# Performance work log

Hardware: AMD Instinct MI355X
Metric: run time of the kernel (lower is better)

## Reference

```python
import jax, jax.numpy as jnp
import numpy as np

MUL = 32            # multiplicity of 0e and 1o irreps
IN_DIM = MUL * 4    # 32 scalars + 32 vectors = 128
SH_DIM = 4          # 1x0e + 1x1o
N_EDGE_FEAT = 128
HIDDEN = 128
W_NUMEL = 4 * MUL * MUL  # 4 CG paths, uvw weights 32x1x32 each
EPS = 1e-5
INV_SQRT3 = 1.0 / np.sqrt(3.0)
PATH_NORM = 1.0 / np.sqrt(2.0 * MUL)  # 2 paths per output irrep, fan-in MUL


def _fc(edge_attr, W1, b1, W2, b2):
    h = jax.nn.relu(edge_attr @ W1 + b1)
    return h @ W2 + b2  # [E, W_NUMEL]


def _tensor_product(x, sh, w):
    # FullyConnectedTensorProduct for (32x0e+32x1o) x (1x0e+1x1o) -> (32x0e+32x1o)
    # CG (real w3j): 0x0->0: 1 ; 0x1->1, 1x0->1, 1x1->0: delta/sqrt(3)
    E = x.shape[0]
    x0 = x[:, :MUL]                      # [E,32]   scalars
    x1 = x[:, MUL:].reshape(E, MUL, 3)   # [E,32,3] vectors
    sh0 = sh[:, 0]                       # [E]
    sh1 = sh[:, 1:4]                     # [E,3]
    wA = w[:, 0 * MUL * MUL:1 * MUL * MUL].reshape(E, MUL, MUL)  # 0e x 0e -> 0e
    wB = w[:, 1 * MUL * MUL:2 * MUL * MUL].reshape(E, MUL, MUL)  # 0e x 1o -> 1o
    wC = w[:, 2 * MUL * MUL:3 * MUL * MUL].reshape(E, MUL, MUL)  # 1o x 0e -> 1o
    wD = w[:, 3 * MUL * MUL:4 * MUL * MUL].reshape(E, MUL, MUL)  # 1o x 1o -> 0e
    out0 = PATH_NORM * (
        jnp.einsum('eu,euw->ew', x0 * sh0[:, None], wA)
        + INV_SQRT3 * jnp.einsum('eui,ei,euw->ew', x1, sh1, wD))
    out1 = PATH_NORM * INV_SQRT3 * (
        jnp.einsum('eu,ei,euw->ewi', x0, sh1, wB)
        + jnp.einsum('eui,euw->ewi', x1 * sh0[:, None, None], wC))
    return jnp.concatenate([out0, out1.reshape(E, MUL * 3)], axis=-1)  # [E,128]


def _batch_norm(x, bn_weight, bn_bias):
    # e3nn-style equivariant BatchNorm (training stats): scalars get mean/var
    # normalization + affine; vectors get norm normalization + scale.
    N = x.shape[0]
    s = x[:, :MUL]                       # [N,32]
    v = x[:, MUL:].reshape(N, MUL, 3)    # [N,32,3]
    s = s - s.mean(axis=0)
    s = s * (jax.lax.rsqrt((s ** 2).mean(axis=0) + EPS) * bn_weight[:MUL]) + bn_bias
    v_norm = jax.lax.rsqrt((v ** 2).mean(axis=-1).mean(axis=0) + EPS)  # [32]
    v = v * (v_norm * bn_weight[MUL:])[None, :, None]
    return jnp.concatenate([s, v.reshape(N, MUL * 3)], axis=-1)


def _forward(node_attr, edge_index, edge_attr, edge_sh,
             W1, b1, W2, b2, bn_weight, bn_bias):
    edge_src, edge_dst = edge_index[0], edge_index[1]
    N = node_attr.shape[0]
    w = _fc(edge_attr, W1, b1, W2, b2)                     # [E, 4096]
    tp = _tensor_product(node_attr[edge_dst], edge_sh, w)  # [E, 128]
    # scatter mean over edge_src
    summed = jax.ops.segment_sum(tp, edge_src, num_segments=N)
    counts = jax.ops.segment_sum(jnp.ones((tp.shape[0],), tp.dtype), edge_src,
                                 num_segments=N)
    out = summed / jnp.maximum(counts, 1.0)[:, None]
    out = out + node_attr                                  # residual (same dim, pad=0)
    return _batch_norm(out, bn_weight, bn_bias)


def setup_inputs() -> dict:
    key = jax.random.key(0)
    ks = jax.random.split(key, 10)
    N, E = 10000, 60000
    node_attr = jax.random.normal(ks[0], (N, IN_DIM), jnp.float32)
    edge_index = jax.random.randint(ks[1], (2, E), 0, N)
    edge_attr = jax.random.normal(ks[2], (E, N_EDGE_FEAT), jnp.float32)
    edge_sh = jax.random.normal(ks[3], (E, SH_DIM), jnp.float32)
    W1 = jax.random.normal(ks[4], (N_EDGE_FEAT, HIDDEN), jnp.float32) / np.sqrt(N_EDGE_FEAT)
    b1 = jnp.zeros((HIDDEN,), jnp.float32)
    W2 = jax.random.normal(ks[5], (HIDDEN, W_NUMEL), jnp.float32) / np.sqrt(HIDDEN)
    b2 = jnp.zeros((W_NUMEL,), jnp.float32)
    bn_weight = jnp.ones((2 * MUL,), jnp.float32)
    bn_bias = jnp.zeros((MUL,), jnp.float32)
    return {"node_attr": node_attr, "edge_index": edge_index,
            "edge_attr": edge_attr, "edge_sh": edge_sh,
            "W1": W1, "b1": b1, "W2": W2, "b2": b2,
            "bn_weight": bn_weight, "bn_bias": bn_bias}


def reference(node_attr, edge_index, edge_attr, edge_sh,
              W1, b1, W2, b2, bn_weight, bn_bias):
    return _forward(node_attr, edge_index, edge_attr, edge_sh,
                    W1, b1, W2, b2, bn_weight, bn_bias)
```

## Files before the change

kernel.cpp:

```cpp
#include <hip/hip_runtime.h>
#include <math.h>

#define EPSV 1e-5f
#define IS3  0.57735026918962576f
#define PNRM 0.125f

typedef __attribute__((ext_vector_type(8)))  short  short8;
typedef __attribute__((ext_vector_type(16))) float  floatx16;

static __device__ inline unsigned short f2bf(float f) {
    unsigned int u = __float_as_uint(f);
    return (unsigned short)((u + 0x7fff + ((u >> 16) & 1)) >> 16);
}
static __device__ inline float bflo(unsigned int u) { return __uint_as_float(u << 16); }
static __device__ inline float bfhi(unsigned int u) { return __uint_as_float(u & 0xffff0000u); }

#define GLD16(gp, lp) __builtin_amdgcn_global_load_lds( \
    (const __attribute__((address_space(1))) unsigned int*)(gp), \
    (__attribute__((address_space(3))) unsigned int*)(lp), 16, 0, 0)

__global__ __launch_bounds__(256) void k0_sw(const float* __restrict__ src,
                                             unsigned short* __restrict__ dst,
                                             int total, int ncShift, int ncMask) {
    int i = blockIdx.x * 256 + threadIdx.x;
    if (i >= total) return;
    int k = i >> ncShift, c = i & ncMask;
    dst[(size_t)(c >> 5) * 4096 + (k >> 3) * 256 + (c & 31) * 8 + (k & 7)] = f2bf(src[i]);
}

__global__ __launch_bounds__(256) void k1_fc(const float* __restrict__ ea,
                                             const unsigned short* __restrict__ W1T,
                                             const float* __restrict__ b1,
                                             const int* __restrict__ ei,
                                             unsigned short* __restrict__ h,
                                             int* __restrict__ deg, int E) {
    __shared__ __align__(16) unsigned short W1s[16384];
    const int tid = threadIdx.x, lane = tid & 63, wv = tid >> 6;
    const int half = lane >> 5, col = lane & 31;
    const int e0 = blockIdx.x * 128;

    if (tid < 128) { int e = e0 + tid; if (e < E) atomicAdd(&deg[ei[e]], 1); }

#pragma unroll
    for (int q = 0; q < 8; ++q) {
        int chunk = wv * 8 + q;
        GLD16((const char*)W1T + chunk * 1024 + lane * 16, (char*)W1s + chunk * 1024);
    }

    int e = e0 + wv * 32 + col; if (e >= E) e = E - 1;
    short8 afr[8];
#pragma unroll
    for (int c = 0; c < 8; ++c) {
        const float4* p = (const float4*)(ea + (size_t)e * 128 + c * 16 + half * 8);
        float4 f0 = p[0], f1 = p[1];
        short8 v;
        v[0] = (short)f2bf(f0.x); v[1] = (short)f2bf(f0.y);
        v[2] = (short)f2bf(f0.z); v[3] = (short)f2bf(f0.w);
        v[4] = (short)f2bf(f1.x); v[5] = (short)f2bf(f1.y);
        v[6] = (short)f2bf(f1.z); v[7] = (short)f2bf(f1.w);
        afr[c] = v;
    }
    __syncthreads();

#pragma unroll
    for (int jt = 0; jt < 4; ++jt) {
        floatx16 d = {0,0,0,0,0,0,0,0,0,0,0,0,0,0,0,0};
#pragma unroll
        for (int c = 0; c < 8; ++c) {
            short8 bf = *(const short8*)((const char*)W1s + jt * 8192 + (2 * c + half) * 512 + col * 16);
            d = __builtin_amdgcn_mfma_f32_32x32x16_bf16(afr[c], bf, d, 0, 0, 0);
        }
        int j = jt * 32 + col;
        float b1v = b1[j];
#pragma unroll
        for (int reg = 0; reg < 16; ++reg) {
            int r = (reg & 3) + 8 * (reg >> 2) + 4 * half;
            int er = e0 + wv * 32 + r;
            if (er < E) {
                float v = d[reg] + b1v;
                v = v > 0.f ? v : 0.f;
                h[(size_t)er * 128 + j] = f2bf(v);
            }
        }
    }
}

__global__ __launch_bounds__(256, 2) void k2_mfma(const unsigned short* __restrict__ h,
                                                  const unsigned short* __restrict__ W2T,
                                                  const float* __restrict__ b2,
                                                  const float* __restrict__ na,
                                                  const int* __restrict__ ei,
                                                  const float* __restrict__ sh,
                                                  float* __restrict__ tp, int E) {
    __shared__ __align__(16) char smem[74752];
    unsigned short* As  = (unsigned short*)smem;
    unsigned short* Bs0 = (unsigned short*)(smem + 16384);
    unsigned short* Bs1 = (unsigned short*)(smem + 32768);
    unsigned short* Ctb = (unsigned short*)(smem + 49152);
    float* shs = (float*)(smem + 73728);
    float* red = (float*)smem;

    const int tid = threadIdx.x, lane = tid & 63, wv = tid >> 6;
    const int half = lane >> 5, col = lane & 31;
    const int ust = wv >> 1, esub = wv & 1;
    const int e0 = blockIdx.x * 64;

    if (tid < 64) {
        int e = e0 + tid; int ec = e < E ? e : E - 1;
        float4 s = *(const float4*)(sh + (size_t)ec * 4);
        *(float4*)&shs[tid * 4] = s;
    }

    for (int idx = tid; idx < 2048; idx += 256) {
        int el = idx & 63, u = idx >> 6;
        int e = e0 + el; int ec = e < E ? e : E - 1;
        int dn = ei[E + ec];
        const float* nar = na + (size_t)dn * 128;
        float x0  = nar[u];
        float x10 = nar[32 + u * 3], x11 = nar[33 + u * 3], x12 = nar[34 + u * 3];
        const float* shr = sh + (size_t)ec * 4;
        float s0 = shr[0], s1 = shr[1], s2 = shr[2], s3 = shr[3];
        int o = u * 64 + el;
        Ctb[0 * 2048 + o] = f2bf(x0 * s0);
        Ctb[1 * 2048 + o] = f2bf(x0);
        Ctb[2 * 2048 + o] = f2bf(x10);
        Ctb[3 * 2048 + o] = f2bf(x11);
        Ctb[4 * 2048 + o] = f2bf(x12);
        Ctb[5 * 2048 + o] = f2bf(IS3 * (x10 * s1 + x11 * s2 + x12 * s3));
    }

#pragma unroll
    for (int q = 0; q < 4; ++q) {
        int t = wv * 4 + q;
        int g = t >> 3;
        int jj = (t & 7) * 64 + lane;
        int e = e0 + g * 32 + (jj & 31); int ec = e < E ? e : E - 1;
        GLD16((const char*)h + (size_t)ec * 256 + (jj >> 5) * 16,
              (char*)As + g * 8192 + (t & 7) * 1024);
    }
#pragma unroll
    for (int q = 0; q < 4; ++q) {
        int chunk = wv * 4 + q;
        GLD16((const char*)W2T + chunk * 1024 + lane * 16, (char*)Bs0 + chunk * 1024);
    }
    __syncthreads();

    short8 afr[8];
#pragma unroll
    for (int c = 0; c < 8; ++c)
        afr[c] = *(const short8*)((const char*)As + esub * 8192 + (2 * c + half) * 512 + col * 16);

    float acc0[16] = {}, accB[16] = {}, accC0[16] = {}, accC1[16] = {}, accC2[16] = {};

    for (int p = 0; p < 64; ++p) {
        if (p < 63) {
            char* dst = ((p + 1) & 1) ? (char*)Bs1 : (char*)Bs0;
#pragma unroll
            for (int q = 0; q < 4; ++q) {
                int chunk = wv * 4 + q;
                GLD16((const char*)W2T + (p + 1) * 16384 + chunk * 1024 + lane * 16,
                      dst + chunk * 1024);
            }
        }
        const int ct = 2 * p + ust;
        const int b = ct >> 5, u = ct & 31;
        const char* bb = ((p & 1) ? (const char*)Bs1 : (const char*)Bs0) + ust * 8192;

        floatx16 d = {0,0,0,0,0,0,0,0,0,0,0,0,0,0,0,0};
#pragma unroll
        for (int c = 0; c < 8; ++c) {
            short8 bf = *(const short8*)(bb + (2 * c + half) * 512 + col * 16);
            d = __builtin_amdgcn_mfma_f32_32x32x16_bf16(afr[c], bf, d, 0, 0, 0);
        }
        float b2v = b2[ct * 32 + col];

        const int elb0 = esub * 32 + half * 4;
        if (b == 0 || b == 3) {
            const unsigned short* tb = Ctb + (b == 0 ? 0 : 5) * 2048;
#pragma unroll
            for (int q = 0; q < 4; ++q) {
                uint2 cv = *(const uint2*)&tb[u * 64 + elb0 + q * 8];
                acc0[q * 4 + 0] += bflo(cv.x) * (d[q * 4 + 0] + b2v);
                acc0[q * 4 + 1] += bfhi(cv.x) * (d[q * 4 + 1] + b2v);
                acc0[q * 4 + 2] += bflo(cv.y) * (d[q * 4 + 2] + b2v);
                acc0[q * 4 + 3] += bfhi(cv.y) * (d[q * 4 + 3] + b2v);
            }
        } else if (b == 1) {
#pragma unroll
            for (int q = 0; q < 4; ++q) {
                uint2 cv = *(const uint2*)&Ctb[1 * 2048 + u * 64 + elb0 + q * 8];
                accB[q * 4 + 0] += bflo(cv.x) * (d[q * 4 + 0] + b2v);
                accB[q * 4 + 1] += bfhi(cv.x) * (d[q * 4 + 1] + b2v);
                accB[q * 4 + 2] += bflo(cv.y) * (d[q * 4 + 2] + b2v);
                accB[q * 4 + 3] += bfhi(cv.y) * (d[q * 4 + 3] + b2v);
            }
        } else {
#pragma unroll
            for (int q = 0; q < 4; ++q) {
                uint2 c0 = *(const uint2*)&Ctb[2 * 2048 + u * 64 + elb0 + q * 8];
                uint2 c1 = *(const uint2*)&Ctb[3 * 2048 + u * 64 + elb0 + q * 8];
                uint2 c2 = *(const uint2*)&Ctb[4 * 2048 + u * 64 + elb0 + q * 8];
#pragma unroll
                for (int rr = 0; rr < 4; ++rr) {
                    float v = d[q * 4 + rr] + b2v;
                    float f0 = (rr == 0) ? bflo(c0.x) : (rr == 1) ? bfhi(c0.x) : (rr == 2) ? bflo(c0.y) : bfhi(c0.y);
                    float f1 = (rr == 0) ? bflo(c1.x) : (rr == 1) ? bfhi(c1.x) : (rr == 2) ? bflo(c1.y) : bfhi(c1.y);
                    float f2 = (rr == 0) ? bflo(c2.x) : (rr == 1) ? bfhi(c2.x) : (rr == 2) ? bflo(c2.y) : bfhi(c2.y);
                    accC0[q * 4 + rr] += f0 * v;
                    accC1[q * 4 + rr] += f1 * v;
                    accC2[q * 4 + rr] += f2 * v;
                }
            }
        }
        __syncthreads();
    }

    if (ust == 1) {
#pragma unroll
        for (int reg = 0; reg < 16; ++reg) {
            red[(((esub * 5 + 0) * 16 + reg) << 6) + lane] = acc0[reg];
            red[(((esub * 5 + 1) * 16 + reg) << 6) + lane] = accB[reg];
            red[(((esub * 5 + 2) * 16 + reg) << 6) + lane] = accC0[reg];
            red[(((esub * 5 + 3) * 16 + reg) << 6) + lane] = accC1[reg];
            red[(((esub * 5 + 4) * 16 + reg) << 6) + lane] = accC2[reg];
        }
    }
    __syncthreads();
    if (ust == 0) {
#pragma unroll
        for (int q = 0; q < 4; ++q) {
#pragma unroll
            for (int rr = 0; rr < 4; ++rr) {
                int reg = q * 4 + rr;
                int el = esub * 32 + q * 8 + half * 4 + rr;
                int e = e0 + el;
                if (e >= E) continue;
                float a0 = acc0[reg] + red[(((esub * 5 + 0) * 16 + reg) << 6) + lane];
                float aB = accB[reg] + red[(((esub * 5 + 1) * 16 + reg) << 6) + lane];
                float c0v = accC0[reg] + red[(((esub * 5 + 2) * 16 + reg) << 6) + lane];
                float c1v = accC1[reg] + red[(((esub * 5 + 3) * 16 + reg) << 6) + lane];
                float c2v = accC2[reg] + red[(((esub * 5 + 4) * 16 + reg) << 6) + lane];
                float4 sv = *(const float4*)&shs[el * 4];
                float* tpe = tp + (size_t)e * 128;
                tpe[col] = PNRM * a0;
                tpe[32 + col * 3 + 0] = PNRM * IS3 * (sv.y * aB + sv.x * c0v);
                tpe[32 + col * 3 + 1] = PNRM * IS3 * (sv.z * aB + sv.x * c1v);
                tpe[32 + col * 3 + 2] = PNRM * IS3 * (sv.w * aB + sv.x * c2v);
            }
        }
    }
}

__global__ __launch_bounds__(1024) void k_scan(const int* __restrict__ deg,
                                               int* __restrict__ rowptr, int N) {
    __shared__ int part[1024];
    const int tid = threadIdx.x;
    const int chunk = (N + 1023) / 1024;
    const int base = tid * chunk;
    int s = 0;
    for (int i = 0; i < chunk; ++i) {
        int n = base + i;
        if (n < N) s += deg[n];
    }
    part[tid] = s;
    __syncthreads();
    for (int off = 1; off < 1024; off <<= 1) {
        int t = 0;
        if (tid >= off) t = part[tid - off];
        __syncthreads();
        if (tid >= off) part[tid] += t;
        __syncthreads();
    }
    int prefix = (tid == 0) ? 0 : part[tid - 1];
    for (int i = 0; i < chunk; ++i) {
        int n = base + i;
        if (n < N) { rowptr[n] = prefix; prefix += deg[n]; }
    }
    if (tid == 0) rowptr[N] = part[1023];
}

__global__ __launch_bounds__(256) void k_fill(const int* __restrict__ ei,
                                              const int* __restrict__ rowptr,
                                              int* __restrict__ cursor,
                                              int* __restrict__ elist, int E) {
    int e = blockIdx.x * 256 + threadIdx.x;
    if (e >= E) return;
    int s = ei[e];
    int pos = rowptr[s] + atomicAdd(&cursor[s], 1);
    elist[pos] = e;
}

__global__ __launch_bounds__(256) void k4_gather(const float* __restrict__ tp,
                                                 const int* __restrict__ rowptr,
                                                 const int* __restrict__ elist,
                                                 const float* __restrict__ na,
                                                 float* __restrict__ pre,
                                                 float* __restrict__ stats, int N) {
    __shared__ float bns[96];
    const int tid = threadIdx.x;
    if (tid < 96) bns[tid] = 0.f;
    __syncthreads();
    const int o = tid & 127, hf = tid >> 7;
    for (int n = blockIdx.x * 2 + hf; n < N; n += gridDim.x * 2) {
        int r0 = rowptr[n], r1 = rowptr[n + 1];
        float s = 0.f;
        for (int j = r0; j < r1; ++j)
            s += tp[(size_t)elist[j] * 128 + o];
        int dg = r1 - r0;
        float cf = (float)(dg > 0 ? dg : 1);
        float v = s / cf + na[(size_t)n * 128 + o];
        pre[(size_t)n * 128 + o] = v;
        if (o < 32) {
            atomicAdd(&bns[o], v);
            atomicAdd(&bns[32 + o], v * v);
        } else {
            atomicAdd(&bns[64 + (o - 32) / 3], v * v);
        }
    }
    __syncthreads();
    if (tid < 96) atomicAdd(&stats[tid], bns[tid]);
}

__global__ __launch_bounds__(256) void k5_bn(const float* __restrict__ pre,
                                             const float* __restrict__ stats,
                                             const float* __restrict__ bnw,
                                             const float* __restrict__ bnb,
                                             float* __restrict__ out, int N) {
    size_t idx = (size_t)blockIdx.x * 256 + threadIdx.x;
    if (idx >= (size_t)N * 128) return;
    int o = (int)(idx & 127);
    float v = pre[idx];
    float invN = 1.f / (float)N;
    if (o < 32) {
        float m   = stats[o] * invN;
        float var = stats[32 + o] * invN - m * m;
        out[idx] = (v - m) * rsqrtf(var + EPSV) * bnw[o] + bnb[o];
    } else {
        int j = (o - 32) / 3;
        float vn = rsqrtf(stats[64 + j] * invN * (1.f / 3.f) + EPSV);
        out[idx] = v * vn * bnw[32 + j];
    }
}

extern "C" void kernel_launch(void* const* d_in, const int* in_sizes, int n_in,
                              void* d_out, int out_size, void* d_ws, size_t ws_size,
                              hipStream_t stream) {
    const float* node_attr  = (const float*)d_in[0];
    const int*   edge_index = (const int*)d_in[1];
    const float* edge_attr  = (const float*)d_in[2];
    const float* edge_sh    = (const float*)d_in[3];
    const float* W1  = (const float*)d_in[4];
    const float* b1  = (const float*)d_in[5];
    const float* W2  = (const float*)d_in[6];
    const float* b2  = (const float*)d_in[7];
    const float* bnw = (const float*)d_in[8];
    const float* bnb = (const float*)d_in[9];

    const int N = in_sizes[0] / 128;
    const int E = in_sizes[1] / 2;

    float* tp     = (float*)d_ws;
    float* pre    = tp + (size_t)E * 128;
    float* stats  = pre + (size_t)N * 128;
    int*   deg    = (int*)(stats + 96);
    int*   cursor = deg + N;
    int*   rowptr = cursor + N;
    int*   elist  = rowptr + N + 1;
    char* pbase = (char*)(elist + E);
    pbase += (16 - ((size_t)pbase & 15)) & 15;
    unsigned short* h   = (unsigned short*)pbase;
    unsigned short* W2T = h + (size_t)E * 128;
    unsigned short* W1T = W2T + (size_t)524288;

    hipMemsetAsync(stats, 0, (96 + 2 * (size_t)N) * sizeof(int), stream);

    k0_sw<<<(128 * 4096 + 255) / 256, 256, 0, stream>>>(W2, W2T, 128 * 4096, 12, 4095);
    k0_sw<<<(128 * 128 + 255) / 256, 256, 0, stream>>>(W1, W1T, 128 * 128, 7, 127);
    k1_fc<<<(E + 127) / 128, 256, 0, stream>>>(edge_attr, W1T, b1, edge_index, h, deg, E);
    k_scan<<<1, 1024, 0, stream>>>(deg, rowptr, N);
    k_fill<<<(E + 255) / 256, 256, 0, stream>>>(edge_index, rowptr, cursor, elist, E);
    k2_mfma<<<(E + 63) / 64, 256, 0, stream>>>(h, W2T, b2, node_attr, edge_index,
                                               edge_sh, tp, E);
    k4_gather<<<256, 256, 0, stream>>>(tp, rowptr, elist, node_attr, pre, stats, N);
    size_t ntot = (size_t)N * 128;
    k5_bn<<<(int)((ntot + 255) / 256), 256, 0, stream>>>(pre, stats, bnw, bnb,
                                                         (float*)d_out, N);
}
```

Before: 317.4 us.

## Stream W2 fragments into registers directly and coalesce weight/hidden stores

The main MFMA kernel stops staging W2 tiles through double-buffered LDS with a per-iteration barrier. Each wave instead loads its B fragments straight from global (L2-resident) memory into registers with a two-deep software pipeline, which cuts LDS from about 73KB to 42KB and drops 64 __syncthreads. The FC kernel stages its output tile in LDS so that h is written as 16-byte rows rather than scattered 2-byte stores, and the weight swizzle kernel now writes its destination contiguously and gathers from the source instead. The cost is more registers for the prefetched fragments and repeated global/L2 reads of W2 by every block.

```diff
diff --git a/kernel.cpp b/kernel.cpp
--- a/kernel.cpp
+++ b/kernel.cpp
@@ -21,11 +21,13 @@
 
 __global__ __launch_bounds__(256) void k0_sw(const float* __restrict__ src,
                                              unsigned short* __restrict__ dst,
-                                             int total, int ncShift, int ncMask) {
+                                             int total, int nc) {
     int i = blockIdx.x * 256 + threadIdx.x;
     if (i >= total) return;
-    int k = i >> ncShift, c = i & ncMask;
-    dst[(size_t)(c >> 5) * 4096 + (k >> 3) * 256 + (c & 31) * 8 + (k & 7)] = f2bf(src[i]);
+    int tile = i >> 12, t = i & 4095;
+    int k = ((t >> 8) << 3) | (t & 7);
+    int c = (tile << 5) | ((t >> 3) & 31);
+    dst[i] = f2bf(src[(size_t)k * nc + c]);
 }
 
 __global__ __launch_bounds__(256) void k1_fc(const float* __restrict__ ea,
@@ -35,6 +37,7 @@
                                              unsigned short* __restrict__ h,
                                              int* __restrict__ deg, int E) {
     __shared__ __align__(16) unsigned short W1s[16384];
+    __shared__ __align__(16) unsigned short outT[5120];
     const int tid = threadIdx.x, lane = tid & 63, wv = tid >> 6;
     const int half = lane >> 5, col = lane & 31;
     const int e0 = blockIdx.x * 128;
@@ -70,18 +73,26 @@
             short8 bf = *(const short8*)((const char*)W1s + jt * 8192 + (2 * c + half) * 512 + col * 16);
             d = __builtin_amdgcn_mfma_f32_32x32x16_bf16(afr[c], bf, d, 0, 0, 0);
         }
-        int j = jt * 32 + col;
-        float b1v = b1[j];
+        float b1v = b1[jt * 32 + col];
 #pragma unroll
         for (int reg = 0; reg < 16; ++reg) {
             int r = (reg & 3) + 8 * (reg >> 2) + 4 * half;
-            int er = e0 + wv * 32 + r;
+            float v = d[reg] + b1v;
+            v = v > 0.f ? v : 0.f;
+            outT[(wv * 32 + r) * 40 + col] = f2bf(v);
+        }
+        __syncthreads();
+#pragma unroll
+        for (int ps = 0; ps < 2; ++ps) {
+            int lin = ps * 256 + tid;
+            int row = lin >> 2, c8 = (lin & 3) * 8;
+            int er = e0 + row;
             if (er < E) {
-                float v = d[reg] + b1v;
-                v = v > 0.f ? v : 0.f;
-                h[(size_t)er * 128 + j] = f2bf(v);
+                short8 v = *(const short8*)&outT[row * 40 + c8];
+                *(short8*)(h + (size_t)er * 128 + jt * 32 + c8) = v;
             }
         }
+        __syncthreads();
     }
 }
 
@@ -92,12 +103,10 @@
                                                   const int* __restrict__ ei,
                                                   const float* __restrict__ sh,
                                                   float* __restrict__ tp, int E) {
-    __shared__ __align__(16) char smem[74752];
+    __shared__ __align__(16) char smem[42240];
     unsigned short* As  = (unsigned short*)smem;
-    unsigned short* Bs0 = (unsigned short*)(smem + 16384);
-    unsigned short* Bs1 = (unsigned short*)(smem + 32768);
-    unsigned short* Ctb = (unsigned short*)(smem + 49152);
-    float* shs = (float*)(smem + 73728);
+    unsigned short* Ctb = (unsigned short*)(smem + 16384);
+    float* shs = (float*)(smem + 40960);
     float* red = (float*)smem;
 
     const int tid = threadIdx.x, lane = tid & 63, wv = tid >> 6;
@@ -138,11 +147,6 @@
         GLD16((const char*)h + (size_t)ec * 256 + (jj >> 5) * 16,
               (char*)As + g * 8192 + (t & 7) * 1024);
     }
-#pragma unroll
-    for (int q = 0; q < 4; ++q) {
-        int chunk = wv * 4 + q;
-        GLD16((const char*)W2T + chunk * 1024 + lane * 16, (char*)Bs0 + chunk * 1024);
-    }
     __syncthreads();
 
     short8 afr[8];
@@ -151,70 +155,75 @@
         afr[c] = *(const short8*)((const char*)As + esub * 8192 + (2 * c + half) * 512 + col * 16);
 
     float acc0[16] = {}, accB[16] = {}, accC0[16] = {}, accC1[16] = {}, accC2[16] = {};
-
-    for (int p = 0; p < 64; ++p) {
-        if (p < 63) {
-            char* dst = ((p + 1) & 1) ? (char*)Bs1 : (char*)Bs0;
-#pragma unroll
-            for (int q = 0; q < 4; ++q) {
-                int chunk = wv * 4 + q;
-                GLD16((const char*)W2T + (p + 1) * 16384 + chunk * 1024 + lane * 16,
-                      dst + chunk * 1024);
-            }
-        }
-        const int ct = 2 * p + ust;
-        const int b = ct >> 5, u = ct & 31;
-        const char* bb = ((p & 1) ? (const char*)Bs1 : (const char*)Bs0) + ust * 8192;
-
-        floatx16 d = {0,0,0,0,0,0,0,0,0,0,0,0,0,0,0,0};
-#pragma unroll
-        for (int c = 0; c < 8; ++c) {
-            short8 bf = *(const short8*)(bb + (2 * c + half) * 512 + col * 16);
-            d = __builtin_amdgcn_mfma_f32_32x32x16_bf16(afr[c], bf, d, 0, 0, 0);
-        }
-        float b2v = b2[ct * 32 + col];
-
-        const int elb0 = esub * 32 + half * 4;
-        if (b == 0 || b == 3) {
-            const unsigned short* tb = Ctb + (b == 0 ? 0 : 5) * 2048;
-#pragma unroll
-            for (int q = 0; q < 4; ++q) {
-                uint2 cv = *(const uint2*)&tb[u * 64 + elb0 + q * 8];
-                acc0[q * 4 + 0] += bflo(cv.x) * (d[q * 4 + 0] + b2v);
-                acc0[q * 4 + 1] += bfhi(cv.x) * (d[q * 4 + 1] + b2v);
-                acc0[q * 4 + 2] += bflo(cv.y) * (d[q * 4 + 2] + b2v);
-                acc0[q * 4 + 3] += bfhi(cv.y) * (d[q * 4 + 3] + b2v);
-            }
-        } else if (b == 1) {
-#pragma unroll
-            for (int q = 0; q < 4; ++q) {
-                uint2 cv = *(const uint2*)&Ctb[1 * 2048 + u * 64 + elb0 + q * 8];
-                accB[q * 4 + 0] += bflo(cv.x) * (d[q * 4 + 0] + b2v);
-                accB[q * 4 + 1] += bfhi(cv.x) * (d[q * 4 + 1] + b2v);
-                accB[q * 4 + 2] += bflo(cv.y) * (d[q * 4 + 2] + b2v);
-                accB[q * 4 + 3] += bfhi(cv.y) * (d[q * 4 + 3] + b2v);
-            }
-        } else {
-#pragma unroll
-            for (int q = 0; q < 4; ++q) {
-                uint2 c0 = *(const uint2*)&Ctb[2 * 2048 + u * 64 + elb0 + q * 8];
-                uint2 c1 = *(const uint2*)&Ctb[3 * 2048 + u * 64 + elb0 + q * 8];
-                uint2 c2 = *(const uint2*)&Ctb[4 * 2048 + u * 64 + elb0 + q * 8];
-#pragma unroll
-                for (int rr = 0; rr < 4; ++rr) {
-                    float v = d[q * 4 + rr] + b2v;
-                    float f0 = (rr == 0) ? bflo(c0.x) : (rr == 1) ? bfhi(c0.x) : (rr == 2) ? bflo(c0.y) : bfhi(c0.y);
-                    float f1 = (rr == 0) ? bflo(c1.x) : (rr == 1) ? bfhi(c1.x) : (rr == 2) ? bflo(c1.y) : bfhi(c1.y);
-                    float f2 = (rr == 0) ? bflo(c2.x) : (rr == 1) ? bfhi(c2.x) : (rr == 2) ? bflo(c2.y) : bfhi(c2.y);
-                    accC0[q * 4 + rr] += f0 * v;
-                    accC1[q * 4 + rr] += f1 * v;
-                    accC2[q * 4 + rr] += f2 * v;
-                }
-            }
-        }
-        __syncthreads();
-    }
-
+    const int elb0 = esub * 32 + half * 4;
+    const unsigned short* bbase = W2T + half * 256 + col * 8;
+
+#define LOADB(p, br, b2r) do {                                         \
+        int _ct = 2 * (p) + ust;                                       \
+        const unsigned short* _bp = bbase + (size_t)_ct * 4096;        \
+        _Pragma("unroll")                                              \
+        for (int _c = 0; _c < 8; ++_c)                                 \
+            (br)[_c] = *(const short8*)(_bp + _c * 512);               \
+        (b2r) = b2[_ct * 32 + col];                                    \
+    } while (0)
+
+#define COMPUTE(p, br, b2v) do {                                                              \
+        const int _ct = 2 * (p) + ust;                                                        \
+        const int _b = _ct >> 5, _u = _ct & 31;                                               \
+        floatx16 d = {0,0,0,0,0,0,0,0,0,0,0,0,0,0,0,0};                                       \
+        _Pragma("unroll")                                                                     \
+        for (int _c = 0; _c < 8; ++_c)                                                        \
+            d = __builtin_amdgcn_mfma_f32_32x32x16_bf16(afr[_c], (br)[_c], d, 0, 0, 0);       \
+        if (_b == 0 || _b == 3) {                                                             \
+            const unsigned short* tb = Ctb + (_b == 0 ? 0 : 5) * 2048;                        \
+            _Pragma("unroll")                                                                 \
+            for (int q = 0; q < 4; ++q) {                                                     \
+                uint2 cv = *(const uint2*)&tb[_u * 64 + elb0 + q * 8];                        \
+                acc0[q * 4 + 0] += bflo(cv.x) * (d[q * 4 + 0] + (b2v));                       \
+                acc0[q * 4 + 1] += bfhi(cv.x) * (d[q * 4 + 1] + (b2v));                       \
+                acc0[q * 4 + 2] += bflo(cv.y) * (d[q * 4 + 2] + (b2v));                       \
+                acc0[q * 4 + 3] += bfhi(cv.y) * (d[q * 4 + 3] + (b2v));                       \
+            }                                                                                 \
+        } else if (_b == 1) {                                                                 \
+            _Pragma("unroll")                                                                 \
+            for (int q = 0; q < 4; ++q) {                                                     \
+                uint2 cv = *(const uint2*)&Ctb[1 * 2048 + _u * 64 + elb0 + q * 8];            \
+                accB[q * 4 + 0] += bflo(cv.x) * (d[q * 4 + 0] + (b2v));                       \
+                accB[q * 4 + 1] += bfhi(cv.x) * (d[q * 4 + 1] + (b2v));                       \
+                accB[q * 4 + 2] += bflo(cv.y) * (d[q * 4 + 2] + (b2v));                       \
+                accB[q * 4 + 3] += bfhi(cv.y) * (d[q * 4 + 3] + (b2v));                       \
+            }                                                                                 \
+        } else {                                                                              \
+            _Pragma("unroll")                                                                 \
+            for (int q = 0; q < 4; ++q) {                                                     \
+                uint2 cu0 = *(const uint2*)&Ctb[2 * 2048 + _u * 64 + elb0 + q * 8];           \
+                uint2 cu1 = *(const uint2*)&Ctb[3 * 2048 + _u * 64 + elb0 + q * 8];           \
+                uint2 cu2 = *(const uint2*)&Ctb[4 * 2048 + _u * 64 + elb0 + q * 8];           \
+                float f0[4] = {bflo(cu0.x), bfhi(cu0.x), bflo(cu0.y), bfhi(cu0.y)};           \
+                float f1[4] = {bflo(cu1.x), bfhi(cu1.x), bflo(cu1.y), bfhi(cu1.y)};           \
+                float f2[4] = {bflo(cu2.x), bfhi(cu2.x), bflo(cu2.y), bfhi(cu2.y)};           \
+                _Pragma("unroll")                                                             \
+                for (int rr = 0; rr < 4; ++rr) {                                              \
+                    float v = d[q * 4 + rr] + (b2v);                                          \
+                    accC0[q * 4 + rr] += f0[rr] * v;                                          \
+                    accC1[q * 4 + rr] += f1[rr] * v;                                          \
+                    accC2[q * 4 + rr] += f2[rr] * v;                                          \
+                }                                                                             \
+            }                                                                                 \
+        }                                                                                     \
+    } while (0)
+
+    short8 bA[8], bB[8];
+    float b2A, b2B;
+    LOADB(0, bA, b2A);
+    for (int p = 0; p < 64; p += 2) {
+        LOADB(p + 1, bB, b2B);
+        COMPUTE(p, bA, b2A);
+        if (p + 2 < 64) LOADB(p + 2, bA, b2A);
+        COMPUTE(p + 1, bB, b2B);
+    }
+
+    __syncthreads();
     if (ust == 1) {
 #pragma unroll
         for (int reg = 0; reg < 16; ++reg) {
@@ -235,8 +244,8 @@
                 int el = esub * 32 + q * 8 + half * 4 + rr;
                 int e = e0 + el;
                 if (e >= E) continue;
-                float a0 = acc0[reg] + red[(((esub * 5 + 0) * 16 + reg) << 6) + lane];
-                float aB = accB[reg] + red[(((esub * 5 + 1) * 16 + reg) << 6) + lane];
+                float a0  = acc0[reg]  + red[(((esub * 5 + 0) * 16 + reg) << 6) + lane];
+                float aB  = accB[reg]  + red[(((esub * 5 + 1) * 16 + reg) << 6) + lane];
                 float c0v = accC0[reg] + red[(((esub * 5 + 2) * 16 + reg) << 6) + lane];
                 float c1v = accC1[reg] + red[(((esub * 5 + 3) * 16 + reg) << 6) + lane];
                 float c2v = accC2[reg] + red[(((esub * 5 + 4) * 16 + reg) << 6) + lane];
@@ -249,6 +258,8 @@
             }
         }
     }
+#undef LOADB
+#undef COMPUTE
 }
 
 __global__ __launch_bounds__(1024) void k_scan(const int* __restrict__ deg,
@@ -374,8 +385,8 @@
 
     hipMemsetAsync(stats, 0, (96 + 2 * (size_t)N) * sizeof(int), stream);
 
-    k0_sw<<<(128 * 4096 + 255) / 256, 256, 0, stream>>>(W2, W2T, 128 * 4096, 12, 4095);
-    k0_sw<<<(128 * 128 + 255) / 256, 256, 0, stream>>>(W1, W1T, 128 * 128, 7, 127);
+    k0_sw<<<(128 * 4096 + 255) / 256, 256, 0, stream>>>(W2, W2T, 128 * 4096, 4096);
+    k0_sw<<<(128 * 128 + 255) / 256, 256, 0, stream>>>(W1, W1T, 128 * 128, 128);
     k1_fc<<<(E + 127) / 128, 256, 0, stream>>>(edge_attr, W1T, b1, edge_index, h, deg, E);
     k_scan<<<1, 1024, 0, stream>>>(deg, rowptr, N);
     k_fill<<<(E + 255) / 256, 256, 0, stream>>>(edge_index, rowptr, cursor, elist, E);
```

Result: faster. 302.9 us (-4.6%).
